# Kernel optimization log

Measured on AMD Instinct MI355X. Metric: run time of the kernel, lower is better.

## Reference

```python
import jax, jax.numpy as jnp
import numpy as np

B, T, D, H = 64, 4096, 256, 341  # hidden = 4*256//3 = 341
TAU, RHO, TV_W = 1.0, 0.3, 0.1
NEG = -1e9
EPS = 1e-6
LN_EPS = 1e-5


def entmax15(x, axis=-1):
    """Exact 1.5-entmax via the sort-based threshold algorithm (Peters et al.)."""
    x = (x - jnp.max(x, axis=axis, keepdims=True)) / 2.0
    xsrt = -jnp.sort(-x, axis=axis)                       # descending
    n = x.shape[axis]
    rho = jnp.arange(1, n + 1, dtype=x.dtype)
    mean = jnp.cumsum(xsrt, axis=axis) / rho
    mean_sq = jnp.cumsum(xsrt * xsrt, axis=axis) / rho
    ss = rho * (mean_sq - mean * mean)
    delta = (1.0 - ss) / rho
    tau = mean - jnp.sqrt(jnp.maximum(delta, 0.0))
    support = jnp.sum((tau <= xsrt).astype(jnp.int32), axis=axis, keepdims=True)
    tau_star = jnp.take_along_axis(tau, support - 1, axis=axis)
    return jnp.square(jnp.maximum(x - tau_star, 0.0))


def setup_inputs() -> dict:
    key = jax.random.key(0)
    k_emb, k_len, k_w1, k_w2 = jax.random.split(key, 4)
    embeddings = jax.random.normal(k_emb, (B, T, D), dtype=jnp.float32)
    # variable-length 0/1 attention mask (lengths in [T//4, T]) -> variable k per row
    lengths = jax.random.randint(k_len, (B,), T // 4, T + 1)
    attn = (jnp.arange(T)[None, :] < lengths[:, None]).astype(jnp.float32)
    ln_gamma = jnp.ones((D,), dtype=jnp.float32)
    ln_beta = jnp.zeros((D,), dtype=jnp.float32)
    W1 = jax.random.normal(k_w1, (D, H), dtype=jnp.float32) / np.sqrt(D)
    b1 = jnp.zeros((H,), dtype=jnp.float32)
    W2 = jax.random.normal(k_w2, (H,), dtype=jnp.float32) / np.sqrt(H)
    b2 = jnp.zeros((), dtype=jnp.float32)
    return {"embeddings": embeddings, "attn": attn, "ln_gamma": ln_gamma,
            "ln_beta": ln_beta, "W1": W1, "b1": b1, "W2": W2, "b2": b2}


def reference(embeddings, attn, ln_gamma, ln_beta, W1, b1, W2, b2):
    # SelectorMLP (dropout off at inference)
    emb = embeddings * attn[..., None]                              # [B,T,D]
    mu = jnp.mean(emb, axis=-1, keepdims=True)
    var = jnp.var(emb, axis=-1, keepdims=True)
    xn = (emb - mu) / jnp.sqrt(var + LN_EPS) * ln_gamma + ln_beta
    hid = jax.nn.gelu(jnp.einsum('btd,dh->bth', xn, W1) + b1, approximate=False)
    scores = jnp.einsum('bth,h->bt', hid, W2) + b2                  # [B,T]
    scores = jnp.where(attn == 0, NEG, scores)

    z = entmax15(scores / TAU, axis=1) * attn                       # soft rationale

    # probabilistic_top_k: gumbel-perturbed variable-k top-k, vectorized
    u = jax.random.uniform(jax.random.key(42), scores.shape, dtype=scores.dtype)
    gumbel = -jnp.log(-jnp.log(u + EPS) + EPS)
    pert = scores * attn + gumbel                                   # [B,T]
    t_eff = jnp.sum(attn, axis=1)                                   # [B]
    k = jnp.clip(jnp.round(RHO * t_eff), 1.0, jnp.maximum(t_eff, 1.0)).astype(jnp.int32)
    srt = -jnp.sort(-pert, axis=1)                                  # descending
    thr = jnp.take_along_axis(srt, (k - 1)[:, None], axis=1)        # k-th largest
    h = (pert >= thr).astype(z.dtype) * attn                        # hard mask

    # straight-through estimator
    g = jax.lax.stop_gradient(h - z) + z

    # total variation regularizer on g within valid region
    dz = jnp.abs(g[:, 1:] - g[:, :-1])
    valid = attn[:, 1:] * attn[:, :-1]
    tv = jnp.mean(jnp.sum(dz * valid, axis=1) / jnp.maximum(jnp.sum(valid, axis=1), 1.0))
    reg = TV_W * tv
    return (z, g, reg)
```

## Files before the change

### kernel.cpp

```cpp
#include <hip/hip_runtime.h>
#include <stdint.h>

#define BB 64
#define TT 4096
#define DD 256
#define HH 341
#define HP 384
#define NEGV (-1e9f)

typedef __attribute__((ext_vector_type(8))) short short8;
typedef __attribute__((ext_vector_type(4))) float f32x4;


__device__ inline float gelu_fast(float x) {
  const float y = fabsf(x) * 0.70710678118654752440f;
  const float t = __builtin_amdgcn_rcpf(fmaf(0.3275911f, y, 1.0f));
  float p = fmaf(1.061405429f, t, -1.453152027f);
  p = fmaf(p, t, 1.421413741f);
  p = fmaf(p, t, -0.284496736f);
  p = fmaf(p, t, 0.254829592f);
  p *= t;
  const float e = __expf(-y * y);
  float er = fmaf(-p, e, 1.0f);
  er = (x < 0.0f) ? -er : er;
  return 0.5f * x * (1.0f + er);
}

__device__ inline uint32_t rotl32(uint32_t x, int d) { return (x << d) | (x >> (32 - d)); }

__device__ inline uint32_t threefry_bits(uint32_t j) {
  const uint32_t K0 = 0u, K1 = 42u;
  const uint32_t K2 = K0 ^ K1 ^ 0x1BD11BDAu;
  uint32_t x0 = 0u, x1 = j;
  x0 += K0; x1 += K1;
#define TF_RND(r) { x0 += x1; x1 = rotl32(x1, r); x1 ^= x0; }
  TF_RND(13) TF_RND(15) TF_RND(26) TF_RND(6)
  x0 += K1; x1 += K2 + 1u;
  TF_RND(17) TF_RND(29) TF_RND(16) TF_RND(24)
  x0 += K2; x1 += K0 + 2u;
  TF_RND(13) TF_RND(15) TF_RND(26) TF_RND(6)
  x0 += K0; x1 += K1 + 3u;
  TF_RND(17) TF_RND(29) TF_RND(16) TF_RND(24)
  x0 += K1; x1 += K2 + 4u;
  TF_RND(13) TF_RND(15) TF_RND(26) TF_RND(6)
  x0 += K2; x1 += K0 + 5u;
#undef TF_RND
  return x0 ^ x1;
}

__device__ inline void bf16split(float x, short& hi, short& lo) {
  uint32_t u = __float_as_uint(x);
  uint32_t h = (u + 0x7FFFu + ((u >> 16) & 1u)) >> 16;
  float rem = x - __uint_as_float(h << 16);
  uint32_t ur = __float_as_uint(rem);
  uint32_t l = (ur + 0x7FFFu + ((ur >> 16) & 1u)) >> 16;
  hi = (short)h; lo = (short)l;
}

__device__ inline float bred_sum(float v, volatile float* tmp, int tid) {
#pragma unroll
  for (int o = 32; o; o >>= 1) v += __shfl_xor(v, o, 64);
  __syncthreads();
  if ((tid & 63) == 0) tmp[tid >> 6] = v;
  __syncthreads();
  return tmp[0] + tmp[1] + tmp[2] + tmp[3];
}

__device__ inline void bred_summax(float& a, float& b, volatile float* tmp, int tid) {
#pragma unroll
  for (int o = 32; o; o >>= 1) { a += __shfl_xor(a, o, 64); b = fmaxf(b, __shfl_xor(b, o, 64)); }
  __syncthreads();
  if ((tid & 63) == 0) { int w2 = (tid >> 6) * 2; tmp[w2] = a; tmp[w2 + 1] = b; }
  __syncthreads();
  a = tmp[0] + tmp[2] + tmp[4] + tmp[6];
  b = fmaxf(fmaxf(tmp[1], tmp[3]), fmaxf(tmp[5], tmp[7]));
}

__device__ inline void bred_sum2(float& a, float& b, volatile float* tmp, int tid) {
#pragma unroll
  for (int o = 32; o; o >>= 1) { a += __shfl_xor(a, o, 64); b += __shfl_xor(b, o, 64); }
  __syncthreads();
  if ((tid & 63) == 0) { int w2 = (tid >> 6) * 2; tmp[w2] = a; tmp[w2 + 1] = b; }
  __syncthreads();
  a = tmp[0] + tmp[2] + tmp[4] + tmp[6];
  b = tmp[1] + tmp[3] + tmp[5] + tmp[7];
}

__device__ inline void bred3_i(int& a, int& b, int& c, volatile int* tmp, int tid) {
#pragma unroll
  for (int o = 32; o; o >>= 1) {
    a += __shfl_xor(a, o, 64);
    b += __shfl_xor(b, o, 64);
    c += __shfl_xor(c, o, 64);
  }
  __syncthreads();
  if ((tid & 63) == 0) { int w3 = (tid >> 6) * 3; tmp[w3] = a; tmp[w3 + 1] = b; tmp[w3 + 2] = c; }
  __syncthreads();
  a = tmp[0] + tmp[3] + tmp[6] + tmp[9];
  b = tmp[1] + tmp[4] + tmp[7] + tmp[10];
  c = tmp[2] + tmp[5] + tmp[8] + tmp[11];
}


__global__ __launch_bounds__(384) void k0_prep(const float* __restrict__ W1,
                                               short* __restrict__ Whi,
                                               short* __restrict__ Wlo,
                                               int* __restrict__ done_ctr) {
  const int k = blockIdx.x;
  const int h = threadIdx.x;
  if (k == 0 && h == 0) *done_ctr = 0;
  float v = (h < HH) ? W1[k * HH + h] : 0.0f;
  short hi, lo;
  bf16split(v, hi, lo);
  Whi[h * DD + k] = hi;
  Wlo[h * DD + k] = lo;
}


__global__ __launch_bounds__(512, 6) void k1_mfma(
    const float* __restrict__ emb, const float* __restrict__ attn,
    const float* __restrict__ gamma, const float* __restrict__ beta,
    const short* __restrict__ Whi, const float* __restrict__ b1,
    const float* __restrict__ W2, const float* __restrict__ b2,
    float* __restrict__ scores) {
  __shared__ short Ahi[8192];
  __shared__ short Alo[8192];

  const int bid = blockIdx.x;
  const int b = bid >> 7;
  const int t0 = (bid & 127) * 32;
  const int tid = threadIdx.x;
  const int w = tid >> 6;
  const int lane = tid & 63;

  if (attn[(size_t)b * TT + t0] == 0.0f) {
    if (tid < 32) scores[(size_t)b * TT + t0 + tid] = NEGV;
    return;
  }

  {
    const int half = lane >> 5;
    const int g = lane & 31;
    const int k0g = g >> 2, qg = g & 3;
    float gg[8], bb[8];
#pragma unroll
    for (int j = 0; j < 8; ++j) { gg[j] = gamma[g * 8 + j]; bb[j] = beta[g * 8 + j]; }

    float a2[2];
    float4 xA2[2], xB2[2];
#pragma unroll
    for (int it = 0; it < 2; ++it) {
      const int il = w * 4 + it * 2 + half;
      const size_t rowoff = (size_t)b * TT + t0 + il;
      a2[it] = attn[rowoff];
      const float* ep = emb + rowoff * DD + g * 8;
      xA2[it] = *(const float4*)ep;
      xB2[it] = *(const float4*)(ep + 4);
    }

#pragma unroll
    for (int it = 0; it < 2; ++it) {
      const int il = w * 4 + it * 2 + half;
      const float a = a2[it];
      float x[8];
      x[0] = xA2[it].x * a; x[1] = xA2[it].y * a; x[2] = xA2[it].z * a; x[3] = xA2[it].w * a;
      x[4] = xB2[it].x * a; x[5] = xB2[it].y * a; x[6] = xB2[it].z * a; x[7] = xB2[it].w * a;
      float s = 0.f, ss = 0.f;
#pragma unroll
      for (int j = 0; j < 8; ++j) { s += x[j]; ss += x[j] * x[j]; }
#pragma unroll
      for (int o = 16; o; o >>= 1) { s += __shfl_xor(s, o, 32); ss += __shfl_xor(ss, o, 32); }
      const float mu = s * (1.0f / DD);
      const float rs = 1.0f / sqrtf(ss * (1.0f / DD) - mu * mu + 1e-5f);

      short8 h8, l8;
#pragma unroll
      for (int j = 0; j < 8; ++j) {
        float y = (x[j] - mu) * rs * gg[j] + bb[j];
        short hi, lo;
        bf16split(y, hi, lo);
        h8[j] = hi; l8[j] = lo;
      }
      const int i15 = il & 15, mt = il >> 4;
      const int slot = mt * 512 + k0g * 64 + qg * 16 + (i15 ^ k0g);
      *(short8*)&Ahi[slot * 8] = h8;
      *(short8*)&Alo[slot * 8] = l8;
    }
  }
  __syncthreads();

  const int r = lane & 15, q = lane >> 4;
  f32x4 acc[3][2];
#pragma unroll
  for (int j = 0; j < 3; ++j)
#pragma unroll
    for (int mt = 0; mt < 2; ++mt) acc[j][mt] = (f32x4){0.f, 0.f, 0.f, 0.f};

  int hb[3];
#pragma unroll
  for (int j = 0; j < 3; ++j) hb[j] = ((w * 3 + j) * 16 + r) * 256 + q * 8;

#pragma unroll
  for (int k0 = 0; k0 < 8; ++k0) {
    short8 ahi[2], alo[2];
#pragma unroll
    for (int mt = 0; mt < 2; ++mt) {
      const int slot = mt * 512 + k0 * 64 + q * 16 + (r ^ k0);
      ahi[mt] = *(const short8*)&Ahi[slot * 8];
      alo[mt] = *(const short8*)&Alo[slot * 8];
    }
#pragma unroll
    for (int j = 0; j < 3; ++j) {
      const short* bp = Whi + hb[j] + k0 * 32;
      short8 bhi = *(const short8*)bp;
      short8 blo = *(const short8*)(bp + HP * DD);
#pragma unroll
      for (int mt = 0; mt < 2; ++mt) {
        acc[j][mt] = __builtin_amdgcn_mfma_f32_16x16x32_bf16(ahi[mt], bhi, acc[j][mt], 0, 0, 0);
        acc[j][mt] = __builtin_amdgcn_mfma_f32_16x16x32_bf16(ahi[mt], blo, acc[j][mt], 0, 0, 0);
        acc[j][mt] = __builtin_amdgcn_mfma_f32_16x16x32_bf16(alo[mt], bhi, acc[j][mt], 0, 0, 0);
      }
    }
  }

  float part[2][4];
#pragma unroll
  for (int mt = 0; mt < 2; ++mt)
#pragma unroll
    for (int rr = 0; rr < 4; ++rr) part[mt][rr] = 0.f;

#pragma unroll
  for (int j = 0; j < 3; ++j) {
    const int h = (w * 3 + j) * 16 + r;
    const float w2v = (h < HH) ? W2[h] : 0.f;
    const float b1v = (h < HH) ? b1[h] : 0.f;
#pragma unroll
    for (int mt = 0; mt < 2; ++mt)
#pragma unroll
      for (int rr = 0; rr < 4; ++rr)
        part[mt][rr] += gelu_fast(acc[j][mt][rr] + b1v) * w2v;
  }

  float sacc[2][4];
#pragma unroll
  for (int mt = 0; mt < 2; ++mt)
#pragma unroll
    for (int rr = 0; rr < 4; ++rr) {
      float v = part[mt][rr];
      v += __shfl_xor(v, 1, 64);
      v += __shfl_xor(v, 2, 64);
      v += __shfl_xor(v, 4, 64);
      v += __shfl_xor(v, 8, 64);
      sacc[mt][rr] = v;
    }

  __syncthreads();
  float* sred = (float*)Ahi;
  if (r == 0) {
#pragma unroll
    for (int mt = 0; mt < 2; ++mt)
#pragma unroll
      for (int rr = 0; rr < 4; ++rr)
        sred[w * 32 + mt * 16 + q * 4 + rr] = sacc[mt][rr];
  }
  __syncthreads();

  if (tid < 32) {
    float sc = b2[0];
#pragma unroll
    for (int ww = 0; ww < 8; ++ww) sc += sred[ww * 32 + tid];
    float a = attn[(size_t)b * TT + t0 + tid];
    scores[(size_t)b * TT + t0 + tid] = (a != 0.f) ? sc : NEGV;
  }
}


__global__ __launch_bounds__(256) void k2_select(
    const float* __restrict__ attn, float* __restrict__ out,
    float* __restrict__ row_tv, int* __restrict__ done_ctr) {
  __shared__ float gs[TT];
  __shared__ float ftmp[8];
  __shared__ int itmp[12];
  __shared__ int is_last;

  const int b = blockIdx.x, tid = threadIdx.x;
  const float* arow = attn + (size_t)b * TT;
  float* zrow = out + (size_t)b * TT;
  float* grow = out + (size_t)BB * TT + (size_t)b * TT;

  float x_loc[16], a_loc[16];
  uint32_t key_loc[16];
  float cnt = 0.0f, mx = -3.4e38f;
#pragma unroll
  for (int i = 0; i < 16; ++i) {
    int t = tid + i * 256;
    float s = grow[t];
    float a = arow[t];
    a_loc[i] = a;
    x_loc[i] = s;
    cnt += a;
    mx = fmaxf(mx, s);
    uint32_t bits = threefry_bits((uint32_t)(b * TT + t));
    float u = __uint_as_float(0x3F800000u | (bits >> 9)) - 1.0f;
    float gum = -logf(1e-6f - logf(u + 1e-6f));
    float pert = (a != 0.0f ? s : 0.0f) + gum;
    uint32_t fb = __float_as_uint(pert);
    uint32_t msk = ((int32_t)fb < 0) ? 0xFFFFFFFFu : 0x80000000u;
    key_loc[i] = fb ^ msk;
  }
  float t_eff = cnt;
  bred_summax(t_eff, mx, ftmp, tid);

#pragma unroll
  for (int i = 0; i < 16; ++i) x_loc[i] = (x_loc[i] - mx) * 0.5f;

  float tau = -1.0f;
  for (int it = 0; it < 18; ++it) {
    float f = 0.0f, g = 0.0f;
#pragma unroll
    for (int i = 0; i < 16; ++i) {
      float d = x_loc[i] - tau;
      if (d > 0.0f) { f = fmaf(d, d, f); g += d; }
    }
    bred_sum2(f, g, ftmp, tid);
    tau = fminf(tau + (f - 1.0f) / (2.0f * g), -0.015625f);
  }

  float kf = rintf(0.3f * t_eff);
  kf = fminf(fmaxf(kf, 1.0f), fmaxf(t_eff, 1.0f));
  int kk = (int)kf;

  uint32_t prefix = 0u;
  for (int bit = 30; bit >= 0; bit -= 2) {
    uint32_t ph = (prefix >> 2) >> bit;
    int c1 = 0, c2 = 0, c3 = 0;
#pragma unroll
    for (int i = 0; i < 16; ++i) {
      uint32_t kb = key_loc[i];
      bool m = (((kb >> 2) >> bit) == ph);
      uint32_t d = (kb >> bit) & 3u;
      c1 += (int)(m && d >= 1u);
      c2 += (int)(m && d >= 2u);
      c3 += (int)(m && d == 3u);
    }
    bred3_i(c1, c2, c3, itmp, tid);
    uint32_t dig;
    if (c3 >= kk) dig = 3u;
    else if (c2 >= kk) { dig = 2u; kk -= c3; }
    else if (c1 >= kk) { dig = 1u; kk -= c2; }
    else { dig = 0u; kk -= c1; }
    prefix |= dig << bit;
  }
  const uint32_t thr = prefix;

#pragma unroll
  for (int i = 0; i < 16; ++i) {
    int t = tid + i * 256;
    float d = x_loc[i] - tau;
    float z = (d > 0.0f) ? d * d : 0.0f;
    z *= a_loc[i];
    float h = (key_loc[i] >= thr) ? a_loc[i] : 0.0f;
    float g = (h - z) + z;
    zrow[t] = z;
    gs[t] = g;
  }
  __syncthreads();

  float tvn = 0.0f, tvd = 0.0f;
#pragma unroll
  for (int i = 0; i < 16; ++i) {
    int t = tid + i * 256;
    grow[t] = gs[t];
    if (t > 0) {
      float valid = arow[t] * arow[t - 1];
      tvn += fabsf(gs[t] - gs[t - 1]) * valid;
      tvd += valid;
    }
  }
  tvn = bred_sum(tvn, ftmp, tid);
  tvd = bred_sum(tvd, ftmp, tid);

  if (tid == 0) {
    __hip_atomic_store(&row_tv[b], tvn / fmaxf(tvd, 1.0f),
                       __ATOMIC_RELEASE, __HIP_MEMORY_SCOPE_AGENT);
    int prev = __hip_atomic_fetch_add(done_ctr, 1,
                                      __ATOMIC_ACQ_REL, __HIP_MEMORY_SCOPE_AGENT);
    is_last = (prev == BB - 1) ? 1 : 0;
  }
  __syncthreads();
  if (is_last && tid < 64) {
    float v = __hip_atomic_load(&row_tv[tid],
                                __ATOMIC_ACQUIRE, __HIP_MEMORY_SCOPE_AGENT);
#pragma unroll
    for (int o = 32; o; o >>= 1) v += __shfl_xor(v, o, 64);
    if (tid == 0) out[2 * BB * TT] = 0.1f * (v * (1.0f / BB));
  }
}


extern "C" void kernel_launch(void* const* d_in, const int* in_sizes, int n_in,
                              void* d_out, int out_size, void* d_ws, size_t ws_size,
                              hipStream_t stream) {
  const float* emb   = (const float*)d_in[0];
  const float* attn  = (const float*)d_in[1];
  const float* gamma = (const float*)d_in[2];
  const float* beta  = (const float*)d_in[3];
  const float* W1    = (const float*)d_in[4];
  const float* b1    = (const float*)d_in[5];
  const float* W2    = (const float*)d_in[6];
  const float* b2    = (const float*)d_in[7];
  float* out = (float*)d_out;

  float* row_tv = (float*)d_ws;
  int* done_ctr = (int*)((char*)d_ws + 256);
  short* Whi = (short*)((char*)d_ws + 512);
  short* Wlo = Whi + HP * DD;

  k0_prep<<<dim3(DD), dim3(HP), 0, stream>>>(W1, Whi, Wlo, done_ctr);
  k1_mfma<<<dim3(BB * TT / 32), dim3(512), 0, stream>>>(
      emb, attn, gamma, beta, Whi, b1, W2, b2, out + (size_t)BB * TT);
  k2_select<<<dim3(BB), dim3(256), 0, stream>>>(attn, out, row_tv, done_ctr);
}
```

Baseline: 616.7 us.

## Enlarge k1 row tile to 64 with 12 waves and prefetch W1 fragments

The MFMA scoring kernel now handles 64 tokens per block with 12 waves. Each wave owns 2 hidden tiles instead of 3 and processes 4 M-tiles, so every global W1 fragment load is reused across twice as many rows. The next k-step's W1 hi/lo fragments are register-prefetched to overlap global latency with the MFMAs. The cost is more LDS per block, a larger cross-wave reduction, and lower occupancy per CU.

```diff
diff --git a/kernel.cpp b/kernel.cpp
--- a/kernel.cpp
+++ b/kernel.cpp
@@ -117,133 +117,151 @@
 }
 
 
-__global__ __launch_bounds__(512, 6) void k1_mfma(
+__global__ __launch_bounds__(768, 3) void k1_mfma(
     const float* __restrict__ emb, const float* __restrict__ attn,
     const float* __restrict__ gamma, const float* __restrict__ beta,
     const short* __restrict__ Whi, const float* __restrict__ b1,
     const float* __restrict__ W2, const float* __restrict__ b2,
     float* __restrict__ scores) {
-  __shared__ short Ahi[8192];
-  __shared__ short Alo[8192];
+  __shared__ short Ahi[16384];
+  __shared__ short Alo[16384];
 
   const int bid = blockIdx.x;
-  const int b = bid >> 7;
-  const int t0 = (bid & 127) * 32;
+  const int b = bid >> 6;
+  const int t0 = (bid & 63) * 64;
   const int tid = threadIdx.x;
   const int w = tid >> 6;
   const int lane = tid & 63;
 
   if (attn[(size_t)b * TT + t0] == 0.0f) {
-    if (tid < 32) scores[(size_t)b * TT + t0 + tid] = NEGV;
+    if (tid < 64) scores[(size_t)b * TT + t0 + tid] = NEGV;
     return;
   }
 
   {
-    const int half = lane >> 5;
-    const int g = lane & 31;
+    const int g = tid & 31;
+    const int rw = tid >> 5;
     const int k0g = g >> 2, qg = g & 3;
     float gg[8], bb[8];
 #pragma unroll
     for (int j = 0; j < 8; ++j) { gg[j] = gamma[g * 8 + j]; bb[j] = beta[g * 8 + j]; }
 
-    float a2[2];
-    float4 xA2[2], xB2[2];
-#pragma unroll
-    for (int it = 0; it < 2; ++it) {
-      const int il = w * 4 + it * 2 + half;
-      const size_t rowoff = (size_t)b * TT + t0 + il;
-      a2[it] = attn[rowoff];
-      const float* ep = emb + rowoff * DD + g * 8;
-      xA2[it] = *(const float4*)ep;
-      xB2[it] = *(const float4*)(ep + 4);
-    }
-
-#pragma unroll
-    for (int it = 0; it < 2; ++it) {
-      const int il = w * 4 + it * 2 + half;
-      const float a = a2[it];
-      float x[8];
-      x[0] = xA2[it].x * a; x[1] = xA2[it].y * a; x[2] = xA2[it].z * a; x[3] = xA2[it].w * a;
-      x[4] = xB2[it].x * a; x[5] = xB2[it].y * a; x[6] = xB2[it].z * a; x[7] = xB2[it].w * a;
-      float s = 0.f, ss = 0.f;
-#pragma unroll
-      for (int j = 0; j < 8; ++j) { s += x[j]; ss += x[j] * x[j]; }
-#pragma unroll
-      for (int o = 16; o; o >>= 1) { s += __shfl_xor(s, o, 32); ss += __shfl_xor(ss, o, 32); }
-      const float mu = s * (1.0f / DD);
-      const float rs = 1.0f / sqrtf(ss * (1.0f / DD) - mu * mu + 1e-5f);
-
-      short8 h8, l8;
-#pragma unroll
-      for (int j = 0; j < 8; ++j) {
-        float y = (x[j] - mu) * rs * gg[j] + bb[j];
-        short hi, lo;
-        bf16split(y, hi, lo);
-        h8[j] = hi; l8[j] = lo;
+    float a3[3];
+    float4 xA3[3], xB3[3];
+#pragma unroll
+    for (int it = 0; it < 3; ++it) {
+      const int row = it * 24 + rw;
+      if (row < 64) {
+        const size_t rowoff = (size_t)b * TT + t0 + row;
+        a3[it] = attn[rowoff];
+        const float* ep = emb + rowoff * DD + g * 8;
+        xA3[it] = *(const float4*)ep;
+        xB3[it] = *(const float4*)(ep + 4);
       }
-      const int i15 = il & 15, mt = il >> 4;
-      const int slot = mt * 512 + k0g * 64 + qg * 16 + (i15 ^ k0g);
-      *(short8*)&Ahi[slot * 8] = h8;
-      *(short8*)&Alo[slot * 8] = l8;
+    }
+
+#pragma unroll
+    for (int it = 0; it < 3; ++it) {
+      const int row = it * 24 + rw;
+      if (row < 64) {
+        const float a = a3[it];
+        float x[8];
+        x[0] = xA3[it].x * a; x[1] = xA3[it].y * a; x[2] = xA3[it].z * a; x[3] = xA3[it].w * a;
+        x[4] = xB3[it].x * a; x[5] = xB3[it].y * a; x[6] = xB3[it].z * a; x[7] = xB3[it].w * a;
+        float s = 0.f, ss = 0.f;
+#pragma unroll
+        for (int j = 0; j < 8; ++j) { s += x[j]; ss += x[j] * x[j]; }
+#pragma unroll
+        for (int o = 16; o; o >>= 1) { s += __shfl_xor(s, o, 32); ss += __shfl_xor(ss, o, 32); }
+        const float mu = s * (1.0f / DD);
+        const float rs = 1.0f / sqrtf(ss * (1.0f / DD) - mu * mu + 1e-5f);
+
+        short8 h8, l8;
+#pragma unroll
+        for (int j = 0; j < 8; ++j) {
+          float y = (x[j] - mu) * rs * gg[j] + bb[j];
+          short hi, lo;
+          bf16split(y, hi, lo);
+          h8[j] = hi; l8[j] = lo;
+        }
+        const int i15 = row & 15, mt = row >> 4;
+        const int slot = mt * 512 + k0g * 64 + qg * 16 + (i15 ^ k0g);
+        *(short8*)&Ahi[slot * 8] = h8;
+        *(short8*)&Alo[slot * 8] = l8;
+      }
     }
   }
   __syncthreads();
 
   const int r = lane & 15, q = lane >> 4;
-  f32x4 acc[3][2];
-#pragma unroll
-  for (int j = 0; j < 3; ++j)
-#pragma unroll
-    for (int mt = 0; mt < 2; ++mt) acc[j][mt] = (f32x4){0.f, 0.f, 0.f, 0.f};
-
-  int hb[3];
-#pragma unroll
-  for (int j = 0; j < 3; ++j) hb[j] = ((w * 3 + j) * 16 + r) * 256 + q * 8;
+  f32x4 acc[2][4];
+#pragma unroll
+  for (int j = 0; j < 2; ++j)
+#pragma unroll
+    for (int mt = 0; mt < 4; ++mt) acc[j][mt] = (f32x4){0.f, 0.f, 0.f, 0.f};
+
+  const int hb0 = ((w * 2 + 0) * 16 + r) * 256 + q * 8;
+  const int hb1 = ((w * 2 + 1) * 16 + r) * 256 + q * 8;
+  const short* __restrict__ Wlo_ = Whi + HP * DD;
+
+  short8 bh0 = *(const short8*)(Whi + hb0);
+  short8 bl0 = *(const short8*)(Wlo_ + hb0);
+  short8 bh1 = *(const short8*)(Whi + hb1);
+  short8 bl1 = *(const short8*)(Wlo_ + hb1);
 
 #pragma unroll
   for (int k0 = 0; k0 < 8; ++k0) {
-    short8 ahi[2], alo[2];
-#pragma unroll
-    for (int mt = 0; mt < 2; ++mt) {
+    short8 nh0, nl0, nh1, nl1;
+    if (k0 < 7) {
+      const int o = (k0 + 1) * 32;
+      nh0 = *(const short8*)(Whi + hb0 + o);
+      nl0 = *(const short8*)(Wlo_ + hb0 + o);
+      nh1 = *(const short8*)(Whi + hb1 + o);
+      nl1 = *(const short8*)(Wlo_ + hb1 + o);
+    }
+    short8 ahi[4], alo[4];
+#pragma unroll
+    for (int mt = 0; mt < 4; ++mt) {
       const int slot = mt * 512 + k0 * 64 + q * 16 + (r ^ k0);
       ahi[mt] = *(const short8*)&Ahi[slot * 8];
       alo[mt] = *(const short8*)&Alo[slot * 8];
     }
 #pragma unroll
-    for (int j = 0; j < 3; ++j) {
-      const short* bp = Whi + hb[j] + k0 * 32;
-      short8 bhi = *(const short8*)bp;
-      short8 blo = *(const short8*)(bp + HP * DD);
-#pragma unroll
-      for (int mt = 0; mt < 2; ++mt) {
-        acc[j][mt] = __builtin_amdgcn_mfma_f32_16x16x32_bf16(ahi[mt], bhi, acc[j][mt], 0, 0, 0);
-        acc[j][mt] = __builtin_amdgcn_mfma_f32_16x16x32_bf16(ahi[mt], blo, acc[j][mt], 0, 0, 0);
-        acc[j][mt] = __builtin_amdgcn_mfma_f32_16x16x32_bf16(alo[mt], bhi, acc[j][mt], 0, 0, 0);
-      }
-    }
-  }
-
-  float part[2][4];
-#pragma unroll
-  for (int mt = 0; mt < 2; ++mt)
+    for (int mt = 0; mt < 4; ++mt) {
+      acc[0][mt] = __builtin_amdgcn_mfma_f32_16x16x32_bf16(ahi[mt], bh0, acc[0][mt], 0, 0, 0);
+      acc[0][mt] = __builtin_amdgcn_mfma_f32_16x16x32_bf16(ahi[mt], bl0, acc[0][mt], 0, 0, 0);
+      acc[0][mt] = __builtin_amdgcn_mfma_f32_16x16x32_bf16(alo[mt], bh0, acc[0][mt], 0, 0, 0);
+    }
+#pragma unroll
+    for (int mt = 0; mt < 4; ++mt) {
+      acc[1][mt] = __builtin_amdgcn_mfma_f32_16x16x32_bf16(ahi[mt], bh1, acc[1][mt], 0, 0, 0);
+      acc[1][mt] = __builtin_amdgcn_mfma_f32_16x16x32_bf16(ahi[mt], bl1, acc[1][mt], 0, 0, 0);
+      acc[1][mt] = __builtin_amdgcn_mfma_f32_16x16x32_bf16(alo[mt], bh1, acc[1][mt], 0, 0, 0);
+    }
+    if (k0 < 7) { bh0 = nh0; bl0 = nl0; bh1 = nh1; bl1 = nl1; }
+  }
+
+  float part[4][4];
+#pragma unroll
+  for (int mt = 0; mt < 4; ++mt)
 #pragma unroll
     for (int rr = 0; rr < 4; ++rr) part[mt][rr] = 0.f;
 
 #pragma unroll
-  for (int j = 0; j < 3; ++j) {
-    const int h = (w * 3 + j) * 16 + r;
+  for (int j = 0; j < 2; ++j) {
+    const int h = (w * 2 + j) * 16 + r;
     const float w2v = (h < HH) ? W2[h] : 0.f;
     const float b1v = (h < HH) ? b1[h] : 0.f;
 #pragma unroll
-    for (int mt = 0; mt < 2; ++mt)
+    for (int mt = 0; mt < 4; ++mt)
 #pragma unroll
       for (int rr = 0; rr < 4; ++rr)
         part[mt][rr] += gelu_fast(acc[j][mt][rr] + b1v) * w2v;
   }
 
-  float sacc[2][4];
-#pragma unroll
-  for (int mt = 0; mt < 2; ++mt)
+  float sacc[4][4];
+#pragma unroll
+  for (int mt = 0; mt < 4; ++mt)
 #pragma unroll
     for (int rr = 0; rr < 4; ++rr) {
       float v = part[mt][rr];
@@ -258,17 +276,17 @@
   float* sred = (float*)Ahi;
   if (r == 0) {
 #pragma unroll
-    for (int mt = 0; mt < 2; ++mt)
+    for (int mt = 0; mt < 4; ++mt)
 #pragma unroll
       for (int rr = 0; rr < 4; ++rr)
-        sred[w * 32 + mt * 16 + q * 4 + rr] = sacc[mt][rr];
-  }
-  __syncthreads();
-
-  if (tid < 32) {
+        sred[w * 64 + mt * 16 + q * 4 + rr] = sacc[mt][rr];
+  }
+  __syncthreads();
+
+  if (tid < 64) {
     float sc = b2[0];
 #pragma unroll
-    for (int ww = 0; ww < 8; ++ww) sc += sred[ww * 32 + tid];
+    for (int ww = 0; ww < 12; ++ww) sc += sred[ww * 64 + tid];
     float a = attn[(size_t)b * TT + t0 + tid];
     scores[(size_t)b * TT + t0 + tid] = (a != 0.f) ? sc : NEGV;
   }
@@ -417,7 +435,7 @@
   short* Wlo = Whi + HP * DD;
 
   k0_prep<<<dim3(DD), dim3(HP), 0, stream>>>(W1, Whi, Wlo, done_ctr);
-  k1_mfma<<<dim3(BB * TT / 32), dim3(512), 0, stream>>>(
+  k1_mfma<<<dim3(BB * TT / 64), dim3(768), 0, stream>>>(
       emb, attn, gamma, beta, Whi, b1, W2, b2, out + (size_t)BB * TT);
   k2_select<<<dim3(BB), dim3(256), 0, stream>>>(attn, out, row_tv, done_ctr);
 }
```

New measurement: 583.7 us. 1.06x faster.
